# Performance work log

Measured on AMD Instinct MI355X. Metric: run time of the kernel, lower is better.

## Reference

```python
import jax, jax.numpy as jnp
import numpy as np
import math

B, S, CZ, H, CH = 1, 384, 128, 4, 32


def setup_inputs() -> dict:
    key = jax.random.key(0)
    ks = jax.random.split(key, 12)
    sd = 0.02
    return {
        "z": jax.random.normal(ks[0], (B, S, S, CZ), dtype=jnp.float32),
        "ln_w": jnp.ones((CZ,), dtype=jnp.float32),
        "ln_b": jnp.zeros((CZ,), dtype=jnp.float32),
        "Wq": jax.random.normal(ks[1], (H * CH, CZ), dtype=jnp.float32) * sd,
        "Wk": jax.random.normal(ks[2], (CH, CZ), dtype=jnp.float32) * sd,
        "Wv": jax.random.normal(ks[3], (CH, CZ), dtype=jnp.float32) * sd,
        "Wb": jax.random.normal(ks[4], (H, CZ), dtype=jnp.float32) * sd,
        "Wg": jax.random.normal(ks[5], (H * CH, CZ), dtype=jnp.float32) * sd,
        "bg": jnp.zeros((H * CH,), dtype=jnp.float32),
        "Wo": jax.random.normal(ks[6], (CZ, H * CH), dtype=jnp.float32) * sd,
        "bo": jnp.zeros((CZ,), dtype=jnp.float32),
    }


def reference(z, ln_w, ln_b, Wq, Wk, Wv, Wb, Wg, bg, Wo, bo):
    b_, s_, _, cz = z.shape
    h = Wb.shape[0]          # n_heads
    ch = Wk.shape[0]         # c_hidden
    # LayerNorm over c_z (eps = 1e-5, torch default)
    mu = jnp.mean(z, axis=-1, keepdims=True)
    var = jnp.mean(jnp.square(z - mu), axis=-1, keepdims=True)
    zn = (z - mu) * jax.lax.rsqrt(var + 1e-5) * ln_w + ln_b
    # projections (starting=True: attend along rows i over key index k)
    q = (zn @ Wq.T).reshape(b_, s_, s_, h, ch)   # [B,I,J,H,C]
    k = zn @ Wk.T                                 # [B,I,K,C] shared across heads
    v = zn @ Wv.T                                 # [B,I,K,C]
    bias = zn @ Wb.T                              # [B,I,J,H]
    g = jax.nn.sigmoid(zn @ Wg.T + bg)            # [B,I,J,H*C]
    scale = 1.0 / math.sqrt(ch)
    logits = jnp.einsum('bijhc,bikc->bihjk', q, k) * scale  # [B,I,H,J,K]
    # NOTE: faithful to source — bias broadcasts along the KEY axis (softmax-invariant)
    logits = logits + jnp.transpose(bias, (0, 1, 3, 2))[..., None]
    w = jax.nn.softmax(logits, axis=-1)           # [B,I,H,J,K]
    o = jnp.einsum('bihjk,bikc->bijhc', w, v).reshape(b_, s_, s_, h * ch)
    o = g * o
    return o @ Wo.T + bo
```

## Files before the change

### kernel.cpp

```cpp
#include <hip/hip_runtime.h>
#include <math.h>


typedef unsigned short u16;
typedef __attribute__((ext_vector_type(8))) short short8;
typedef __attribute__((ext_vector_type(4))) short short4v;
typedef __attribute__((ext_vector_type(4))) float float4v;

union U8 { short8 s; u16 h[8]; };
union U4 { short4v s; u16 h[4]; };

__device__ __forceinline__ float bf2f(u16 x){
    unsigned v = ((unsigned)x) << 16;
    float f; __builtin_memcpy(&f, &v, 4);
    return f;
}
__device__ __forceinline__ u16 f2bf(float f){
    unsigned v; __builtin_memcpy(&v, &f, 4);
    unsigned r = (v + 0x7FFFu + ((v >> 16) & 1u)) >> 16;
    return (u16)r;
}
__device__ __forceinline__ short8 pack8f_s(const float* p, float s){
    const float4 a = ((const float4*)p)[0];
    const float4 b = ((const float4*)p)[1];
    U8 u;
    u.h[0]=f2bf(a.x*s); u.h[1]=f2bf(a.y*s); u.h[2]=f2bf(a.z*s); u.h[3]=f2bf(a.w*s);
    u.h[4]=f2bf(b.x*s); u.h[5]=f2bf(b.y*s); u.h[6]=f2bf(b.z*s); u.h[7]=f2bf(b.w*s);
    return u.s;
}

__global__ __launch_bounds__(256) void k0a_wconv(
    const float* __restrict__ Wq, const float* __restrict__ Wk,
    const float* __restrict__ Wv, const float* __restrict__ Wg,
    u16* __restrict__ Wbf)
{
    const int i = blockIdx.x * 256 + threadIdx.x;
    const int e = i * 8;
    const int n = e >> 7, c0 = e & 127;
    const float* src; float s = 1.f;
    if (n < 128)      { src = Wq + n*128 + c0; s = 0.17677669529663689f; }
    else if (n < 160) { src = Wk + (n-128)*128 + c0; }
    else if (n < 192) { src = Wv + (n-160)*128 + c0; }
    else              { src = Wg + (n-192)*128 + c0; }
    *(short8*)(Wbf + e) = pack8f_s(src, s);
}

__global__ __launch_bounds__(256) void k0b_wconv(
    const float* __restrict__ Wo, u16* __restrict__ WoBf)
{
    const int e = (blockIdx.x * 256 + threadIdx.x) * 8;
    *(short8*)(WoBf + e) = pack8f_s(Wo + e, 1.f);
}

__global__ __launch_bounds__(256) void k1_ln_proj(
    const float* __restrict__ z, const float* __restrict__ lnw, const float* __restrict__ lnb,
    const u16* __restrict__ Wbf, const float* __restrict__ bg,
    u16* __restrict__ Qbuf, u16* __restrict__ KVbuf, u16* __restrict__ Gbuf)
{
    __shared__ __align__(16) u16 zn[64][136];
    const int tid = threadIdx.x;
    const long rowg0 = (long)blockIdx.x * 64;

    {
        const int r = tid >> 2, p = tid & 3;
        const float* src = z + (rowg0 + r) * 128 + p * 32;
        float x[32];
        #pragma unroll
        for (int q = 0; q < 8; q++){
            const float4 v = ((const float4*)src)[q];
            x[q*4+0]=v.x; x[q*4+1]=v.y; x[q*4+2]=v.z; x[q*4+3]=v.w;
        }
        float s = 0.f, ss = 0.f;
        #pragma unroll
        for (int t = 0; t < 32; t++){ s += x[t]; ss += x[t]*x[t]; }
        s += __shfl_xor(s, 1);  ss += __shfl_xor(ss, 1);
        s += __shfl_xor(s, 2);  ss += __shfl_xor(ss, 2);
        const float mean = s * (1.f/128.f);
        const float var  = ss * (1.f/128.f) - mean*mean;
        const float rstd = rsqrtf(var + 1e-5f);
        #pragma unroll
        for (int t = 0; t < 32; t++){
            const int c = p*32 + t;
            zn[r][c] = f2bf((x[t]-mean)*rstd*lnw[c] + lnb[c]);
        }
    }
    __syncthreads();

    const int lane = tid & 63, wave = tid >> 6;
    const int l15 = lane & 15, quad = lane >> 4;

    short8 ZN[4][4];
    #pragma unroll
    for (int m = 0; m < 4; m++)
        #pragma unroll
        for (int ks = 0; ks < 4; ks++)
            ZN[m][ks] = *(const short8*)&zn[m*16 + l15][ks*32 + quad*8];

    #pragma unroll
    for (int g = 0; g < 5; g++){
        const int nt = wave*5 + g;
        const u16* wp = Wbf + (nt*16 + l15)*128 + quad*8;
        short8 WF[4];
        #pragma unroll
        for (int ks = 0; ks < 4; ks++) WF[ks] = *(const short8*)(wp + ks*32);
        const int n0 = nt*16 + quad*4;
        #pragma unroll
        for (int m = 0; m < 4; m++){
            float4v c = {0.f,0.f,0.f,0.f};
            #pragma unroll
            for (int ks = 0; ks < 4; ks++)
                c = __builtin_amdgcn_mfma_f32_16x16x32_bf16(WF[ks], ZN[m][ks], c, 0, 0, 0);
            const long row = rowg0 + m*16 + l15;
            if (nt < 8){
                U4 u;
                #pragma unroll
                for (int r = 0; r < 4; r++) u.h[r] = f2bf(c[r]);
                *(short4v*)(Qbuf + row*128 + n0) = u.s;
            } else if (nt < 10){
                U4 u;
                #pragma unroll
                for (int r = 0; r < 4; r++) u.h[r] = f2bf(c[r]);
                *(short4v*)(KVbuf + row*64 + (n0 - 128)) = u.s;
            } else if (nt < 12){
                U4 u;
                #pragma unroll
                for (int r = 0; r < 4; r++) u.h[r] = f2bf(c[r]);
                *(short4v*)(KVbuf + row*64 + (n0 - 160) + 32) = u.s;
            } else {
                const float4 b4 = *(const float4*)&bg[n0 - 192];
                U4 u;
                u.h[0] = f2bf(1.f/(1.f + __expf(-(c[0] + b4.x))));
                u.h[1] = f2bf(1.f/(1.f + __expf(-(c[1] + b4.y))));
                u.h[2] = f2bf(1.f/(1.f + __expf(-(c[2] + b4.z))));
                u.h[3] = f2bf(1.f/(1.f + __expf(-(c[3] + b4.w))));
                *(short4v*)(Gbuf + row*128 + (n0 - 192)) = u.s;
            }
        }
    }
}

__global__ __launch_bounds__(256, 2) void k2_attn(
    const u16* __restrict__ KVbuf, const u16* __restrict__ Gbuf, u16* __restrict__ QObuf)
{
    __shared__ __align__(16) u16 Ks[384][40];
    __shared__ __align__(16) u16 Vt[32][392];
    __shared__ __align__(16) u16 Pb[4][16][200];
    const int i = blockIdx.x >> 2, h = blockIdx.x & 3;
    const int tid = threadIdx.x;
    {
        const u16* kvsrc = KVbuf + (long)i * 384 * 64;
        for (int idx = tid; idx < 384*8; idx += 256){
            const int k = idx >> 3, c8 = idx & 7;
            U8 d; d.s = *(const short8*)(kvsrc + k*64 + c8*8);
            if (c8 < 4) *(short8*)&Ks[k][c8*8] = d.s;
            else {
                const int c0 = (c8 - 4) * 8;
                #pragma unroll
                for (int jj = 0; jj < 8; jj++) Vt[c0 + jj][k] = d.h[jj];
            }
        }
    }
    __syncthreads();

    const int lane = tid & 63, wave = tid >> 6;
    const int l15 = lane & 15, quad = lane >> 4;
    const u16* qbase = QObuf + (long)i * 384 * 128 + h * 32;
    const u16* gbase = Gbuf  + (long)i * 384 * 128 + h * 32;
    u16* obase = QObuf + (long)i * 384 * 128 + h * 32;

    for (int t = 0; t < 6; t++){
        const int j0 = (wave*6 + t) * 16;
        const short8 aq = *(const short8*)(qbase + (long)(j0 + l15)*128 + quad*8);
        float4v acc[24];
        #pragma unroll
        for (int kt = 0; kt < 24; kt++){
            const short8 bk = *(const short8*)&Ks[kt*16 + l15][quad*8];
            float4v zero = {0.f,0.f,0.f,0.f};
            acc[kt] = __builtin_amdgcn_mfma_f32_16x16x32_bf16(aq, bk, zero, 0, 0, 0);
        }
        float inv[4];
        #pragma unroll
        for (int r = 0; r < 4; r++){
            float mx = -1e30f;
            #pragma unroll
            for (int kt = 0; kt < 24; kt++) mx = fmaxf(mx, acc[kt][r]);
            mx = fmaxf(mx, __shfl_xor(mx, 1));
            mx = fmaxf(mx, __shfl_xor(mx, 2));
            mx = fmaxf(mx, __shfl_xor(mx, 4));
            mx = fmaxf(mx, __shfl_xor(mx, 8));
            float sum = 0.f;
            #pragma unroll
            for (int kt = 0; kt < 24; kt++){ acc[kt][r] = __expf(acc[kt][r] - mx); sum += acc[kt][r]; }
            sum += __shfl_xor(sum, 1);
            sum += __shfl_xor(sum, 2);
            sum += __shfl_xor(sum, 4);
            sum += __shfl_xor(sum, 8);
            inv[r] = 1.f / sum;
        }
        float4v oacc[2] = {{0.f,0.f,0.f,0.f},{0.f,0.f,0.f,0.f}};
        #pragma unroll
        for (int kt = 0; kt < 12; kt++)
            #pragma unroll
            for (int r = 0; r < 4; r++)
                Pb[wave][quad*4 + r][kt*16 + l15] = f2bf(acc[kt][r]);
        #pragma unroll
        for (int kk = 0; kk < 6; kk++){
            const short8 ap = *(const short8*)&Pb[wave][l15][kk*32 + quad*8];
            #pragma unroll
            for (int ct = 0; ct < 2; ct++){
                const short8 bv = *(const short8*)&Vt[ct*16 + l15][kk*32 + quad*8];
                oacc[ct] = __builtin_amdgcn_mfma_f32_16x16x32_bf16(ap, bv, oacc[ct], 0, 0, 0);
            }
        }
        #pragma unroll
        for (int kt = 12; kt < 24; kt++)
            #pragma unroll
            for (int r = 0; r < 4; r++)
                Pb[wave][quad*4 + r][(kt-12)*16 + l15] = f2bf(acc[kt][r]);
        #pragma unroll
        for (int kk = 6; kk < 12; kk++){
            const short8 ap = *(const short8*)&Pb[wave][l15][(kk-6)*32 + quad*8];
            #pragma unroll
            for (int ct = 0; ct < 2; ct++){
                const short8 bv = *(const short8*)&Vt[ct*16 + l15][kk*32 + quad*8];
                oacc[ct] = __builtin_amdgcn_mfma_f32_16x16x32_bf16(ap, bv, oacc[ct], 0, 0, 0);
            }
        }
        #pragma unroll
        for (int ct = 0; ct < 2; ct++){
            const int c = ct*16 + l15;
            #pragma unroll
            for (int r = 0; r < 4; r++){
                const int row = j0 + quad*4 + r;
                const float gv = bf2f(gbase[(long)row*128 + c]);
                obase[(long)row*128 + c] = f2bf(gv * (oacc[ct][r] * inv[r]));
            }
        }
    }
}

__global__ __launch_bounds__(256) void k3_outproj(
    const u16* __restrict__ Obuf, const u16* __restrict__ WoBf, const float* __restrict__ bo,
    float* __restrict__ out)
{
    const int tid = threadIdx.x, lane = tid & 63, wave = tid >> 6;
    const int l15 = lane & 15, quad = lane >> 4;
    const long row0 = (long)blockIdx.x * 64;
    short8 WF[2][4];
    #pragma unroll
    for (int g = 0; g < 2; g++){
        const u16* wp = WoBf + ((wave*2 + g)*16 + l15)*128 + quad*8;
        #pragma unroll
        for (int ks = 0; ks < 4; ks++) WF[g][ks] = *(const short8*)(wp + ks*32);
    }
    #pragma unroll
    for (int m = 0; m < 4; m++){
        short8 OF[4];
        const u16* ap = Obuf + (row0 + m*16 + l15)*128 + quad*8;
        #pragma unroll
        for (int ks = 0; ks < 4; ks++) OF[ks] = *(const short8*)(ap + ks*32);
        #pragma unroll
        for (int g = 0; g < 2; g++){
            float4v c = {0.f,0.f,0.f,0.f};
            #pragma unroll
            for (int ks = 0; ks < 4; ks++)
                c = __builtin_amdgcn_mfma_f32_16x16x32_bf16(WF[g][ks], OF[ks], c, 0, 0, 0);
            const int n0 = (wave*2 + g)*16 + quad*4;
            const float4 b4 = *(const float4*)&bo[n0];
            const long row = row0 + m*16 + l15;
            float4 o4;
            o4.x = c[0] + b4.x; o4.y = c[1] + b4.y;
            o4.z = c[2] + b4.z; o4.w = c[3] + b4.w;
            *(float4*)(out + row*128 + n0) = o4;
        }
    }
}

extern "C" void kernel_launch(void* const* d_in, const int* in_sizes, int n_in,
                              void* d_out, int out_size, void* d_ws, size_t ws_size,
                              hipStream_t stream)
{
    (void)in_sizes; (void)n_in; (void)out_size; (void)ws_size;
    const float* z   = (const float*)d_in[0];
    const float* lnw = (const float*)d_in[1];
    const float* lnb = (const float*)d_in[2];
    const float* Wq  = (const float*)d_in[3];
    const float* Wk  = (const float*)d_in[4];
    const float* Wv  = (const float*)d_in[5];
    const float* Wg  = (const float*)d_in[7];
    const float* bg  = (const float*)d_in[8];
    const float* Wo  = (const float*)d_in[9];
    const float* bo  = (const float*)d_in[10];

    u16* Qbuf = (u16*)d_ws;
    u16* KV   = Qbuf + 147456L*128;
    u16* Gbuf = (u16*)d_out;
    u16* Wbf  = Gbuf + 147456L*128;
    u16* WoBf = KV;

    k0a_wconv<<<dim3(20), dim3(256), 0, stream>>>(Wq, Wk, Wv, Wg, Wbf);
    k1_ln_proj<<<dim3(2304), dim3(256), 0, stream>>>(z, lnw, lnb, Wbf, bg,
                                                     Qbuf, KV, Gbuf);
    k2_attn<<<dim3(1536), dim3(256), 0, stream>>>(KV, Gbuf, Qbuf);
    k0b_wconv<<<dim3(8), dim3(256), 0, stream>>>(Wo, WoBf);
    k3_outproj<<<dim3(2304), dim3(256), 0, stream>>>(Qbuf, WoBf, bo, (float*)d_out);
}
```

Baseline: 335.9 us.

## Raise attention occupancy: read K from global, shrink P buffer, use exp2

The attention kernel stops staging K in shared memory and reads K fragments straight from global memory. It also cuts the per-wave P staging buffer to a quarter of the keys at a time and raises launch bounds to 4 blocks per CU. The softmax switches to the native v_exp_f32 (exp2), with log2(e) folded into the Q weight scale. The aim is less LDS use and higher occupancy, at the cost of repeated global/L2 reads of K and more LDS round trips for P.

```diff
diff --git a/kernel.cpp b/kernel.cpp
--- a/kernel.cpp
+++ b/kernel.cpp
@@ -19,6 +19,10 @@
     unsigned v; __builtin_memcpy(&v, &f, 4);
     unsigned r = (v + 0x7FFFu + ((v >> 16) & 1u)) >> 16;
     return (u16)r;
+}
+__device__ __forceinline__ float exp2_fast(float x){
+    float r; asm("v_exp_f32 %0, %1" : "=v"(r) : "v"(x));
+    return r;
 }
 __device__ __forceinline__ short8 pack8f_s(const float* p, float s){
     const float4 a = ((const float4*)p)[0];
@@ -38,7 +42,7 @@
     const int e = i * 8;
     const int n = e >> 7, c0 = e & 127;
     const float* src; float s = 1.f;
-    if (n < 128)      { src = Wq + n*128 + c0; s = 0.17677669529663689f; }
+    if (n < 128)      { src = Wq + n*128 + c0; s = 0.17677669529663689f * 1.4426950408889634f; }
     else if (n < 160) { src = Wk + (n-128)*128 + c0; }
     else if (n < 192) { src = Wv + (n-160)*128 + c0; }
     else              { src = Wg + (n-192)*128 + c0; }
@@ -139,25 +143,21 @@
     }
 }
 
-__global__ __launch_bounds__(256, 2) void k2_attn(
+__global__ __launch_bounds__(256, 4) void k2_attn(
     const u16* __restrict__ KVbuf, const u16* __restrict__ Gbuf, u16* __restrict__ QObuf)
 {
-    __shared__ __align__(16) u16 Ks[384][40];
     __shared__ __align__(16) u16 Vt[32][392];
-    __shared__ __align__(16) u16 Pb[4][16][200];
+    __shared__ __align__(16) u16 Pb[4][16][104];
     const int i = blockIdx.x >> 2, h = blockIdx.x & 3;
     const int tid = threadIdx.x;
+    const u16* kvsrc = KVbuf + (long)i * 384 * 64;
     {
-        const u16* kvsrc = KVbuf + (long)i * 384 * 64;
-        for (int idx = tid; idx < 384*8; idx += 256){
-            const int k = idx >> 3, c8 = idx & 7;
-            U8 d; d.s = *(const short8*)(kvsrc + k*64 + c8*8);
-            if (c8 < 4) *(short8*)&Ks[k][c8*8] = d.s;
-            else {
-                const int c0 = (c8 - 4) * 8;
-                #pragma unroll
-                for (int jj = 0; jj < 8; jj++) Vt[c0 + jj][k] = d.h[jj];
-            }
+        for (int idx = tid; idx < 384*4; idx += 256){
+            const int k = idx >> 2, c8 = idx & 3;
+            U8 d; d.s = *(const short8*)(kvsrc + k*64 + 32 + c8*8);
+            const int c0 = c8 * 8;
+            #pragma unroll
+            for (int jj = 0; jj < 8; jj++) Vt[c0 + jj][k] = d.h[jj];
         }
     }
     __syncthreads();
@@ -167,6 +167,7 @@
     const u16* qbase = QObuf + (long)i * 384 * 128 + h * 32;
     const u16* gbase = Gbuf  + (long)i * 384 * 128 + h * 32;
     u16* obase = QObuf + (long)i * 384 * 128 + h * 32;
+    const u16* kfrag = kvsrc + (long)l15 * 64 + quad * 8;
 
     for (int t = 0; t < 6; t++){
         const int j0 = (wave*6 + t) * 16;
@@ -174,7 +175,7 @@
         float4v acc[24];
         #pragma unroll
         for (int kt = 0; kt < 24; kt++){
-            const short8 bk = *(const short8*)&Ks[kt*16 + l15][quad*8];
+            const short8 bk = *(const short8*)(kfrag + kt*1024);
             float4v zero = {0.f,0.f,0.f,0.f};
             acc[kt] = __builtin_amdgcn_mfma_f32_16x16x32_bf16(aq, bk, zero, 0, 0, 0);
         }
@@ -190,7 +191,7 @@
             mx = fmaxf(mx, __shfl_xor(mx, 8));
             float sum = 0.f;
             #pragma unroll
-            for (int kt = 0; kt < 24; kt++){ acc[kt][r] = __expf(acc[kt][r] - mx); sum += acc[kt][r]; }
+            for (int kt = 0; kt < 24; kt++){ acc[kt][r] = exp2_fast(acc[kt][r] - mx); sum += acc[kt][r]; }
             sum += __shfl_xor(sum, 1);
             sum += __shfl_xor(sum, 2);
             sum += __shfl_xor(sum, 4);
@@ -199,31 +200,23 @@
         }
         float4v oacc[2] = {{0.f,0.f,0.f,0.f},{0.f,0.f,0.f,0.f}};
         #pragma unroll
-        for (int kt = 0; kt < 12; kt++)
-            #pragma unroll
-            for (int r = 0; r < 4; r++)
-                Pb[wave][quad*4 + r][kt*16 + l15] = f2bf(acc[kt][r]);
-        #pragma unroll
-        for (int kk = 0; kk < 6; kk++){
-            const short8 ap = *(const short8*)&Pb[wave][l15][kk*32 + quad*8];
-            #pragma unroll
-            for (int ct = 0; ct < 2; ct++){
-                const short8 bv = *(const short8*)&Vt[ct*16 + l15][kk*32 + quad*8];
-                oacc[ct] = __builtin_amdgcn_mfma_f32_16x16x32_bf16(ap, bv, oacc[ct], 0, 0, 0);
+        for (int cc = 0; cc < 4; cc++){
+            #pragma unroll
+            for (int j = 0; j < 6; j++){
+                const int kt = cc*6 + j;
+                #pragma unroll
+                for (int r = 0; r < 4; r++)
+                    Pb[wave][quad*4 + r][j*16 + l15] = f2bf(acc[kt][r]);
             }
-        }
-        #pragma unroll
-        for (int kt = 12; kt < 24; kt++)
-            #pragma unroll
-            for (int r = 0; r < 4; r++)
-                Pb[wave][quad*4 + r][(kt-12)*16 + l15] = f2bf(acc[kt][r]);
-        #pragma unroll
-        for (int kk = 6; kk < 12; kk++){
-            const short8 ap = *(const short8*)&Pb[wave][l15][(kk-6)*32 + quad*8];
-            #pragma unroll
-            for (int ct = 0; ct < 2; ct++){
-                const short8 bv = *(const short8*)&Vt[ct*16 + l15][kk*32 + quad*8];
-                oacc[ct] = __builtin_amdgcn_mfma_f32_16x16x32_bf16(ap, bv, oacc[ct], 0, 0, 0);
+            #pragma unroll
+            for (int kj = 0; kj < 3; kj++){
+                const int kk = cc*3 + kj;
+                const short8 ap = *(const short8*)&Pb[wave][l15][kj*32 + quad*8];
+                #pragma unroll
+                for (int ct = 0; ct < 2; ct++){
+                    const short8 bv = *(const short8*)&Vt[ct*16 + l15][kk*32 + quad*8];
+                    oacc[ct] = __builtin_amdgcn_mfma_f32_16x16x32_bf16(ap, bv, oacc[ct], 0, 0, 0);
+                }
             }
         }
         #pragma unroll
```

New measurement: 459.2 us. 1.37x slower.
